# Optimization experiments

Hardware: AMD Instinct MI355X
Metric: run time of the kernel (lower is better)

Reference implementation:

```python
import jax, jax.numpy as jnp
import numpy as np

B, Q, DIN, DOUT = 1, 1024, 4096, 4096
H, G, HD = 32, 8, 128          # heads, kv groups, head_dim; group_size = H // G
PREV = 3072                     # cached KV length
MAXPOS = 4096                   # rope table length (>= PREV + Q)
START = PREV


def _rope_tables(max_pos, head_dim):
    half = head_dim // 2
    inv_freq = 1.0 / (10000.0 ** (jnp.arange(half, dtype=jnp.float32) / half))
    ang = jnp.arange(max_pos, dtype=jnp.float32)[:, None] * inv_freq[None, :]
    ang = jnp.concatenate([ang, ang], axis=-1)  # [max_pos, head_dim]
    return jnp.cos(ang), jnp.sin(ang)


def apply_rope(x, cos, sin, start_pos):
    # x: [b, h, s, d]; rotate-half RoPE with absolute positions start_pos..start_pos+s
    s, d = x.shape[2], x.shape[3]
    c = cos[start_pos:start_pos + s]  # [s, d] (start_pos is a Python int)
    sn = sin[start_pos:start_pos + s]
    x1, x2 = x[..., : d // 2], x[..., d // 2:]
    rotated = jnp.concatenate([-x2, x1], axis=-1)
    return x * c + rotated * sn


def setup_inputs() -> dict:
    key = jax.random.key(0)
    ks = jax.random.split(key, 7)
    x = jax.random.normal(ks[0], (B, Q, DIN), dtype=jnp.float32)
    cos, sin = _rope_tables(MAXPOS, HD)
    # causal mask: query at abs position START+i may attend kv position j <= START+i
    qpos = START + jnp.arange(Q)
    kpos = jnp.arange(START + Q)
    mask = (kpos[None, :] > qpos[:, None])[None, None]  # [1,1,Q,KV], True = masked
    prev_k = jax.random.normal(ks[1], (B, G, PREV, HD), dtype=jnp.float32)
    prev_v = jax.random.normal(ks[2], (B, G, PREV, HD), dtype=jnp.float32)
    sc = 0.02
    Wq = jax.random.normal(ks[3], (DIN, DOUT), dtype=jnp.float32) * sc
    Wk = jax.random.normal(ks[4], (DIN, G * HD), dtype=jnp.float32) * sc
    Wv = jax.random.normal(ks[5], (DIN, G * HD), dtype=jnp.float32) * sc
    Wo = jax.random.normal(ks[6], (DOUT, DOUT), dtype=jnp.float32) * sc
    return dict(x=x, mask=mask, cos=cos, sin=sin, start_pos=START,
                prev_k=prev_k, prev_v=prev_v, Wq=Wq, Wk=Wk, Wv=Wv, Wo=Wo)


def reference(x, mask, cos, sin, start_pos, prev_k, prev_v, Wq, Wk, Wv, Wo):
    b, s, _ = x.shape
    gs = H // G  # group_size
    q = (x @ Wq).reshape(b, s, H, HD).transpose(0, 2, 1, 3)   # [b,H,s,hd]
    k = (x @ Wk).reshape(b, s, G, HD).transpose(0, 2, 1, 3)   # [b,G,s,hd]
    v = (x @ Wv).reshape(b, s, G, HD).transpose(0, 2, 1, 3)
    q = apply_rope(q, cos, sin, start_pos)
    k = apply_rope(k, cos, sin, start_pos)
    keys = jnp.concatenate([prev_k, k], axis=2)    # [b,G,KV,hd]
    values = jnp.concatenate([prev_v, v], axis=2)
    # grouped attention (equivalent to repeat_interleave of K/V over group_size)
    qg = q.reshape(b, G, gs, s, HD)
    scores = jnp.einsum('bgnqd,bgkd->bgnqk', qg, keys)        # [b,G,gs,s,KV]
    scores = jnp.where(mask[:, :, None], -jnp.inf, scores)
    attn = jax.nn.softmax(scores / np.sqrt(HD).astype(np.float32), axis=-1)
    ctx = jnp.einsum('bgnqk,bgkd->bgnqd', attn, values)       # [b,G,gs,s,hd]
    ctx = ctx.reshape(b, H, s, HD).transpose(0, 2, 1, 3).reshape(b, s, DOUT)
    out = ctx @ Wo
    return (out, keys, values)
```

## Files before the change

### kernel.cpp

```cpp
#include <hip/hip_runtime.h>
#include <hip/hip_bf16.h>

typedef unsigned short u16;
typedef unsigned int u32;
typedef __attribute__((ext_vector_type(4))) float f32x4;
typedef __attribute__((ext_vector_type(16))) float f32x16;
typedef __attribute__((ext_vector_type(8))) __bf16 bf16x8;
typedef __attribute__((ext_vector_type(4))) u16 u16x4;
typedef __attribute__((ext_vector_type(8))) u16 u16x8;
typedef __attribute__((ext_vector_type(4))) u32 u32x4;

#define START_POS 3072
#define NKV 4096
#define HD_ 128
#define SEQ 1024
#define DIN_ 4096
#define DQKV 6144

__device__ __forceinline__ void gll16(const void* g, void* l) {
  __builtin_amdgcn_global_load_lds((const __attribute__((address_space(1))) u32*)g,
                                   (__attribute__((address_space(3))) u32*)l, 16, 0, 0);
}
__device__ __forceinline__ u16 f2bf(float f) {
  u32 u = __builtin_bit_cast(u32, f);
  return (u16)((u + 0x7fffu + ((u >> 16) & 1u)) >> 16);
}
__device__ __forceinline__ float bf2f(u16 u) {
  u32 x = (u32)u << 16;
  return __builtin_bit_cast(float, x);
}
__device__ __forceinline__ u32 pack2bf(float a, float b) {
  __hip_bfloat162 t = __float22bfloat162_rn(float2{a, b});
  u32 u; __builtin_memcpy(&u, &t, 4);
  return u;
}
__device__ __forceinline__ f32x4 mfma16(bf16x8 a, bf16x8 b, f32x4 c) {
  return __builtin_amdgcn_mfma_f32_16x16x32_bf16(a, b, c, 0, 0, 0);
}
__device__ __forceinline__ f32x16 mfma32(bf16x8 a, bf16x8 b, f32x16 c) {
  return __builtin_amdgcn_mfma_f32_32x32x16_bf16(a, b, c, 0, 0, 0);
}

__global__ __launch_bounds__(256) void wtrans(const float* __restrict__ W,
    u16* __restrict__ Wt, int N, int ntn, int row_off)
{
  __shared__ float T[64][68];
  int bid = blockIdx.x;
  int nt = bid % ntn, kt = bid / ntn;
  int t = threadIdx.x;
  int kl = t >> 4, nl4 = (t & 15) << 2;
#pragma unroll
  for (int r = 0; r < 4; r++) {
    int row = r * 16 + kl;
    f32x4 v = *(const f32x4*)(W + (size_t)(kt * 64 + row) * N + nt * 64 + nl4);
    T[row][nl4] = v[0]; T[row][nl4 + 1] = v[1]; T[row][nl4 + 2] = v[2]; T[row][nl4 + 3] = v[3];
  }
  __syncthreads();
  int nl = t >> 2, k0 = (t & 3) << 4;
  u16x8 lo, hi;
#pragma unroll
  for (int j = 0; j < 8; j++) lo[j] = f2bf(T[k0 + j][nl]);
#pragma unroll
  for (int j = 0; j < 8; j++) hi[j] = f2bf(T[k0 + 8 + j][nl]);
  u16* dst = Wt + (size_t)(row_off + nt * 64 + nl) * 4096 + kt * 64 + k0;
  *(u16x8*)dst = lo;
  *(u16x8*)(dst + 8) = hi;
}

__global__ __launch_bounds__(256) void cvt_bf16(const float* __restrict__ src,
    u16* __restrict__ dst, int n4)
{
  int i = blockIdx.x * 256 + threadIdx.x;
  if (i >= n4) return;
  f32x4 v = *(const f32x4*)(src + (size_t)i * 4);
  u16x4 o;
#pragma unroll
  for (int j = 0; j < 4; j++) o[j] = f2bf(v[j]);
  *(u16x4*)(dst + (size_t)i * 4) = o;
}

__global__ __launch_bounds__(256) void gemm_bt(
    const u16* __restrict__ A, const u16* __restrict__ Bt,
    float* __restrict__ C, int N, int K, int nbx)
{
  __shared__ u16 As[2 * 128 * 64];
  __shared__ u16 Bs[2 * 64 * 64];
  int nwg = (int)gridDim.x;
  int orig = blockIdx.x;
  int q8 = nwg >> 3, r8 = nwg & 7;
  int xcd = orig & 7, jj = orig >> 3;
  int wgid = (xcd < r8 ? xcd * (q8 + 1) : r8 * (q8 + 1) + (xcd - r8) * q8) + jj;
  int by = wgid / nbx, bx = wgid % nbx;
  int tid = threadIdx.x, lane = tid & 63, wid = tid >> 6;
  int wr = wid >> 1, wc = wid & 1;
  int c = lane & 15, hh = lane >> 4;
  int srow = lane >> 3;
  int schunk = ((lane & 7) ^ srow) << 3;
  const u16* aS0 = A + (size_t)(by * 128 + wid * 32 + srow) * K + schunk;
  const u16* bS0 = Bt + (size_t)(bx * 64 + wid * 16 + srow) * K + schunk;

#define GSTAGE(buf, kk) do { \
  _Pragma("unroll") \
  for (int r = 0; r < 4; r++) \
    gll16(aS0 + (size_t)r * 8 * K + (kk), As + (buf) * 8192 + (wid * 32 + r * 8) * 64); \
  _Pragma("unroll") \
  for (int r = 0; r < 2; r++) \
    gll16(bS0 + (size_t)r * 8 * K + (kk), Bs + (buf) * 4096 + (wid * 16 + r * 8) * 64); \
} while (0)

  f32x4 acc[4][2] = {};
  int nk = K >> 6;
  int cur = 0;
  int rsl = c & 7;
  GSTAGE(0, 0);
  __syncthreads();
  for (int kt = 0; kt < nk; kt++) {
    if (kt + 1 < nk) GSTAGE(cur ^ 1, (kt + 1) * 64);
    const u16* Ab = As + cur * 8192;
    const u16* Bb = Bs + cur * 4096;
#pragma unroll
    for (int kk = 0; kk < 2; kk++) {
      int slot = ((kk * 4 + hh) ^ rsl) * 8;
      bf16x8 af[4], bf[2];
#pragma unroll
      for (int i = 0; i < 4; i++)
        af[i] = *(const bf16x8*)(Ab + (wr * 64 + i * 16 + c) * 64 + slot);
#pragma unroll
      for (int i = 0; i < 2; i++)
        bf[i] = *(const bf16x8*)(Bb + (wc * 32 + i * 16 + c) * 64 + slot);
      __builtin_amdgcn_s_setprio(1);
#pragma unroll
      for (int mi = 0; mi < 4; mi++)
#pragma unroll
        for (int ni = 0; ni < 2; ni++)
          acc[mi][ni] = mfma16(af[mi], bf[ni], acc[mi][ni]);
      __builtin_amdgcn_s_setprio(0);
    }
    __syncthreads();
    cur ^= 1;
  }
#undef GSTAGE
  int row0 = by * 128 + wr * 64 + hh * 4;
  int col0 = bx * 64 + wc * 32 + c;
#pragma unroll
  for (int mi = 0; mi < 4; mi++)
#pragma unroll
    for (int ni = 0; ni < 2; ni++)
#pragma unroll
      for (int i = 0; i < 4; i++)
        C[(size_t)(row0 + mi * 16 + i) * N + col0 + ni * 16] = acc[mi][ni][i];
}

__global__ __launch_bounds__(256) void rope_q(const float* __restrict__ qkv,
    const float* __restrict__ cosb, const float* __restrict__ sinb, u16* __restrict__ qb)
{
  const float C2 = 0.12751744f;
  int tid = blockIdx.x * 256 + threadIdx.x;
  int dq = tid & 15, h = (tid >> 4) & 31, s = tid >> 9;
  int d = dq << 2;
  const float* base = qkv + (size_t)s * DQKV + h * HD_ + d;
  f32x4 a = *(const f32x4*)base;
  f32x4 b2 = *(const f32x4*)(base + 64);
  f32x4 cc = *(const f32x4*)(cosb + (size_t)(START_POS + s) * HD_ + d);
  f32x4 sn = *(const f32x4*)(sinb + (size_t)(START_POS + s) * HD_ + d);
  u16x4 o1, o2;
#pragma unroll
  for (int i = 0; i < 4; i++) {
    o1[i] = f2bf((a[i] * cc[i] - b2[i] * sn[i]) * C2);
    o2[i] = f2bf((b2[i] * cc[i] + a[i] * sn[i]) * C2);
  }
  u16* dst = qb + ((size_t)h * SEQ + s) * HD_ + d;
  *(u16x4*)dst = o1;
  *(u16x4*)(dst + 64) = o2;
}

__global__ __launch_bounds__(256) void rope_k(const float* __restrict__ qkv,
    const float* __restrict__ cosb, const float* __restrict__ sinb,
    float* __restrict__ keys, u16* __restrict__ kbb)
{
  int tid = blockIdx.x * 256 + threadIdx.x;
  int dq = tid & 15, g = (tid >> 4) & 7, s = tid >> 7;
  int d = dq << 2;
  const float* base = qkv + (size_t)s * DQKV + DIN_ + g * HD_ + d;
  f32x4 a = *(const f32x4*)base;
  f32x4 b2 = *(const f32x4*)(base + 64);
  f32x4 cc = *(const f32x4*)(cosb + (size_t)(START_POS + s) * HD_ + d);
  f32x4 sn = *(const f32x4*)(sinb + (size_t)(START_POS + s) * HD_ + d);
  f32x4 o1, o2;
  u16x4 p1, p2;
#pragma unroll
  for (int i = 0; i < 4; i++) {
    o1[i] = a[i] * cc[i] - b2[i] * sn[i];
    o2[i] = b2[i] * cc[i] + a[i] * sn[i];
    p1[i] = f2bf(o1[i]);
    p2[i] = f2bf(o2[i]);
  }
  size_t off = ((size_t)g * NKV + START_POS + s) * HD_ + d;
  *(f32x4*)(keys + off) = o1;
  *(f32x4*)(keys + off + 64) = o2;
  *(u16x4*)(kbb + off) = p1;
  *(u16x4*)(kbb + off + 64) = p2;
}

__global__ __launch_bounds__(256) void copy_vnew(const float* __restrict__ qkv,
    float* __restrict__ values)
{
  int tid = blockIdx.x * 256 + threadIdx.x;
  int dq = tid & 31, g = (tid >> 5) & 7, s = tid >> 8;
  int d = dq << 2;
  f32x4 v = *(const f32x4*)(qkv + (size_t)s * DQKV + DIN_ + 1024 + g * HD_ + d);
  *(f32x4*)(values + ((size_t)g * NKV + START_POS + s) * HD_ + d) = v;
}

__global__ __launch_bounds__(256) void prev_copy(const float* __restrict__ pk,
    const float* __restrict__ pv, float* __restrict__ keys, float* __restrict__ values,
    u16* __restrict__ kbb)
{
  int idx = blockIdx.x * 256 + threadIdx.x;
  int d4 = idx & 31;
  int rest = idx >> 5;
  int p = rest % 3072, g = rest / 3072;
  f32x4 kq = *(const f32x4*)(pk + (size_t)idx * 4);
  f32x4 vq = *(const f32x4*)(pv + (size_t)idx * 4);
  size_t off = ((size_t)g * NKV + p) * HD_ + d4 * 4;
  *(f32x4*)(keys + off) = kq;
  *(f32x4*)(values + off) = vq;
  u16x4 kb4;
#pragma unroll
  for (int i = 0; i < 4; i++) kb4[i] = f2bf(kq[i]);
  *(u16x4*)(kbb + off) = kb4;
}

__global__ __launch_bounds__(256) void vtrans(const float* __restrict__ pv,
    const float* __restrict__ qkv, u16* __restrict__ vT)
{
  __shared__ float T[64][68];
  int bid = blockIdx.x;
  int dt = bid & 1, pt = (bid >> 1) & 63, g = bid >> 7;
  int t = threadIdx.x;
  int pl = t >> 4, dl4 = (t & 15) << 2;
#pragma unroll
  for (int r = 0; r < 4; r++) {
    int row = r * 16 + pl;
    int pos = pt * 64 + row;
    f32x4 v;
    if (pos < START_POS)
      v = *(const f32x4*)(pv + ((size_t)g * START_POS + pos) * HD_ + dt * 64 + dl4);
    else
      v = *(const f32x4*)(qkv + (size_t)(pos - START_POS) * DQKV + 5120 + g * HD_ + dt * 64 + dl4);
    T[row][dl4] = v[0]; T[row][dl4 + 1] = v[1]; T[row][dl4 + 2] = v[2]; T[row][dl4 + 3] = v[3];
  }
  __syncthreads();
  int dl = t >> 2, p0 = (t & 3) << 4;
  u16x8 lo, hi;
#pragma unroll
  for (int j = 0; j < 8; j++) lo[j] = f2bf(T[p0 + j][dl]);
#pragma unroll
  for (int j = 0; j < 8; j++) hi[j] = f2bf(T[p0 + 8 + j][dl]);
  u16* dst = vT + ((size_t)g * HD_ + dt * 64 + dl) * NKV + pt * 64 + p0;
  *(u16x8*)dst = lo;
  *(u16x8*)(dst + 8) = hi;
}

__global__ __launch_bounds__(256, 2) void attn_fwd(
    const u16* __restrict__ qb, const u16* __restrict__ kb,
    const u16* __restrict__ vT, u16* __restrict__ Op, float* __restrict__ Ml)
{
  __shared__ u16 Ks[2 * 32 * 128];
  __shared__ u16 Vs[2 * 128 * 32];
  int bid = blockIdx.x;
  int g = bid & 7, j = bid >> 3;
  int sp = j >> 5, jj = j & 31;
  int h = g * 4 + (jj >> 3), qt = jj & 7;
  int tid = threadIdx.x, lane = tid & 63, w = tid >> 6;
  int c32 = lane & 31, h8 = lane >> 5;
  int qw0 = qt * 128 + w * 32;
  bf16x8 Qf[8];
#pragma unroll
  for (int dc = 0; dc < 8; dc++)
    Qf[dc] = *(const bf16x8*)(qb + ((size_t)(h * 1024 + qw0 + c32)) * 128 + dc * 16 + h8 * 8);
  f32x16 O0 = {}, O1 = {}, O2 = {}, O3 = {};
  float Mx = -1e30f, Ls = 0.f;
  int T = 100 + 4 * qt;
  int t0 = (sp * T) >> 2;
  int t1 = ((sp + 1) * T) >> 2;

#define STAGE_KV(tt, bo) do { \
  _Pragma("unroll") \
  for (int r = 0; r < 2; r++) { \
    int s = r * 256 + w * 64 + lane; \
    int krow = s >> 4, sl = s & 15; \
    gll16(kb + ((size_t)(g * 4096 + (tt) * 32 + krow)) * 128 + (sl ^ (krow & 7)) * 8, \
          Ks + (bo) + (r * 256 + w * 64) * 8); \
    int d = s >> 2, sl2 = s & 3; \
    gll16(vT + ((size_t)(g * 128 + d)) * 4096 + (tt) * 32 + (sl2 ^ ((d >> 1) & 3)) * 8, \
          Vs + (bo) + (r * 256 + w * 64) * 8); \
  } \
} while (0)

  int cur = 0;
  STAGE_KV(t0, 0);
  __syncthreads();
  int vxr = (c32 >> 1) & 3;
  for (int t = t0; t < t1; t++) {
    if (t + 1 < t1) STAGE_KV(t + 1, (cur ^ 1) * 4096);
    const u16* Kb = Ks + cur * 4096;
    const u16* Vb = Vs + cur * 4096;
    f32x16 S0 = {}, Sb = {};
    __builtin_amdgcn_s_setprio(1);
#pragma unroll
    for (int dc = 0; dc < 8; dc += 2) {
      int sxA = (2 * dc + h8) ^ (c32 & 7);
      int sxB = (2 * dc + 2 + h8) ^ (c32 & 7);
      bf16x8 kA = *(const bf16x8*)(Kb + (size_t)c32 * 128 + sxA * 8);
      bf16x8 kB = *(const bf16x8*)(Kb + (size_t)c32 * 128 + sxB * 8);
      S0 = mfma32(kA, Qf[dc], S0);
      Sb = mfma32(kB, Qf[dc + 1], Sb);
    }
    __builtin_amdgcn_s_setprio(0);
#pragma unroll
    for (int r = 0; r < 16; r++) S0[r] += Sb[r];
    if (t * 32 + 31 > START_POS + qw0) {
      int qa = START_POS + qw0 + c32;
#pragma unroll
      for (int r = 0; r < 16; r++) {
        int kvo = t * 32 + (r & 3) + 8 * (r >> 2) + 4 * h8;
        if (kvo > qa) S0[r] = -1e30f;
      }
    }
    float tm[16];
#pragma unroll
    for (int r = 0; r < 16; r++) tm[r] = S0[r];
#pragma unroll
    for (int sft = 8; sft >= 1; sft >>= 1)
#pragma unroll
      for (int r = 0; r < sft; r++) tm[r] = fmaxf(tm[r], tm[r + sft]);
    float full = fmaxf(tm[0], __shfl_xor(tm[0], 32));
    if (!__all(full <= Mx + 8.0f)) {
      float Mn = fmaxf(Mx, full);
      float al = exp2f(Mx - Mn);
      Mx = Mn;
      Ls *= al;
#pragma unroll
      for (int r = 0; r < 16; r++) { O0[r] *= al; O1[r] *= al; O2[r] *= al; O3[r] *= al; }
    }
#pragma unroll
    for (int r = 0; r < 16; r++) S0[r] = exp2f(S0[r] - Mx);
    float ts[16];
#pragma unroll
    for (int r = 0; r < 16; r++) ts[r] = S0[r];
#pragma unroll
    for (int sft = 8; sft >= 1; sft >>= 1)
#pragma unroll
      for (int r = 0; r < sft; r++) ts[r] = ts[r] + ts[r + sft];
    Ls += ts[0] + __shfl_xor(ts[0], 32);
    u32 pk0[8], x0[8];
#pragma unroll
    for (int m = 0; m < 8; m++) pk0[m] = pack2bf(S0[2 * m], S0[2 * m + 1]);
#pragma unroll
    for (int m = 0; m < 8; m++) x0[m] = __shfl_xor(pk0[m], 32);
    bf16x8 pbf[2];
    {
      u32x4 f0 = { h8 ? x0[2] : pk0[0], h8 ? x0[3] : pk0[1],
                   h8 ? pk0[2] : x0[0], h8 ? pk0[3] : x0[1] };
      u32x4 f1 = { h8 ? x0[6] : pk0[4], h8 ? x0[7] : pk0[5],
                   h8 ? pk0[6] : x0[4], h8 ? pk0[7] : x0[5] };
      pbf[0] = __builtin_bit_cast(bf16x8, f0);
      pbf[1] = __builtin_bit_cast(bf16x8, f1);
    }
    __builtin_amdgcn_s_setprio(1);
#pragma unroll
    for (int kc = 0; kc < 2; kc++) {
      int sv = 2 * kc + h8;
      int sx = (sv ^ vxr) * 8;
      {
        bf16x8 vf = *(const bf16x8*)(Vb + (size_t)(0 * 32 + c32) * 32 + sx);
        O0 = mfma32(vf, pbf[kc], O0);
      }
      {
        bf16x8 vf = *(const bf16x8*)(Vb + (size_t)(1 * 32 + c32) * 32 + sx);
        O1 = mfma32(vf, pbf[kc], O1);
      }
      {
        bf16x8 vf = *(const bf16x8*)(Vb + (size_t)(2 * 32 + c32) * 32 + sx);
        O2 = mfma32(vf, pbf[kc], O2);
      }
      {
        bf16x8 vf = *(const bf16x8*)(Vb + (size_t)(3 * 32 + c32) * 32 + sx);
        O3 = mfma32(vf, pbf[kc], O3);
      }
    }
    __builtin_amdgcn_s_setprio(0);
    __syncthreads();
    cur ^= 1;
  }
#undef STAGE_KV
  {
    u16* Orow = Op + (size_t)sp * 4194304 + (size_t)(qw0 + c32) * 4096 + h * 128;
#pragma unroll
    for (int a = 0; a < 4; a++) {
      u16x4 o0, o1, o2, o3;
#pragma unroll
      for (int b = 0; b < 4; b++) {
        o0[b] = f2bf(O0[4 * a + b]); o1[b] = f2bf(O1[4 * a + b]);
        o2[b] = f2bf(O2[4 * a + b]); o3[b] = f2bf(O3[4 * a + b]);
      }
      int d0 = 8 * a + 4 * h8;
      *(u16x4*)(Orow + d0) = o0;
      *(u16x4*)(Orow + 32 + d0) = o1;
      *(u16x4*)(Orow + 64 + d0) = o2;
      *(u16x4*)(Orow + 96 + d0) = o3;
    }
    if (h8 == 0) {
      float* mp = Ml + ((size_t)(sp * 32 + h) * 1024 + qw0 + c32) * 2;
      mp[0] = Mx; mp[1] = Ls;
    }
  }
}

__global__ __launch_bounds__(256) void attn_combine(const u16* __restrict__ Op,
    const float* __restrict__ Ml, u16* __restrict__ ctxb)
{
  int idx = blockIdx.x * 256 + threadIdx.x;
  int q = idx >> 10, c4 = idx & 1023;
  int col = c4 * 4, h = col >> 7;
  float m[4], l[4];
#pragma unroll
  for (int s = 0; s < 4; s++) {
    const float* mp = Ml + ((size_t)(s * 32 + h) * 1024 + q) * 2;
    m[s] = mp[0]; l[s] = mp[1];
  }
  float M = fmaxf(fmaxf(m[0], m[1]), fmaxf(m[2], m[3]));
  float wgt[4];
  float den = 0.f;
#pragma unroll
  for (int s = 0; s < 4; s++) { wgt[s] = exp2f(m[s] - M); den += l[s] * wgt[s]; }
  float inv = 1.0f / den;
  float acc[4] = {0.f, 0.f, 0.f, 0.f};
#pragma unroll
  for (int s = 0; s < 4; s++) {
    u16x4 raw = *(const u16x4*)(Op + (size_t)s * 4194304 + (size_t)q * 4096 + col);
#pragma unroll
    for (int i = 0; i < 4; i++) acc[i] += bf2f(raw[i]) * wgt[s];
  }
  u16x4 o;
#pragma unroll
  for (int i = 0; i < 4; i++) o[i] = f2bf(acc[i] * inv);
  *(u16x4*)(ctxb + (size_t)q * 4096 + col) = o;
}

extern "C" void kernel_launch(void* const* d_in, const int* in_sizes, int n_in,
                              void* d_out, int out_size, void* d_ws, size_t ws_size,
                              hipStream_t stream) {
  const float* x      = (const float*)d_in[0];
  const float* cosb   = (const float*)d_in[2];
  const float* sinb   = (const float*)d_in[3];
  const float* prev_k = (const float*)d_in[5];
  const float* prev_v = (const float*)d_in[6];
  const float* Wq     = (const float*)d_in[7];
  const float* Wk     = (const float*)d_in[8];
  const float* Wv     = (const float*)d_in[9];
  const float* Wo     = (const float*)d_in[10];

  u16* Wt_proj = (u16*)d_ws;
  u16* Wt_out  = Wt_proj + (size_t)6144 * 4096;
  u16* xb      = Wt_out + (size_t)4096 * 4096;
  float* qkv   = (float*)(xb + (size_t)1024 * 4096);
  u16* qb      = (u16*)(qkv + (size_t)1024 * 6144);
  u16* kbb     = qb + (size_t)32 * 1024 * 128;
  u16* vT      = kbb + (size_t)8 * 4096 * 128;
  u16* ctxb    = vT + (size_t)8 * 4096 * 128;
  u16* Op   = (u16*)d_ws;
  float* Ml = qkv;

  float* outp   = (float*)d_out;
  float* keys   = outp + (size_t)4194304;
  float* values = outp + (size_t)8388608;

  wtrans<<<4096, 256, 0, stream>>>(Wq, Wt_proj, 4096, 64, 0);
  wtrans<<<1024, 256, 0, stream>>>(Wk, Wt_proj, 1024, 16, 4096);
  wtrans<<<1024, 256, 0, stream>>>(Wv, Wt_proj, 1024, 16, 5120);
  wtrans<<<4096, 256, 0, stream>>>(Wo, Wt_out, 4096, 64, 0);
  cvt_bf16<<<4096, 256, 0, stream>>>(x, xb, 1048576);

  gemm_bt<<<768, 256, 0, stream>>>(xb, Wt_proj, qkv, 6144, 4096, 96);

  rope_q<<<2048, 256, 0, stream>>>(qkv, cosb, sinb, qb);
  rope_k<<<512, 256, 0, stream>>>(qkv, cosb, sinb, keys, kbb);
  copy_vnew<<<1024, 256, 0, stream>>>(qkv, values);
  prev_copy<<<3072, 256, 0, stream>>>(prev_k, prev_v, keys, values, kbb);
  vtrans<<<1024, 256, 0, stream>>>(prev_v, qkv, vT);

  attn_fwd<<<1024, 256, 0, stream>>>(qb, kbb, vT, Op, Ml);
  attn_combine<<<4096, 256, 0, stream>>>(Op, Ml, ctxb);

  gemm_bt<<<512, 256, 0, stream>>>(ctxb, Wt_out, outp, 4096, 4096, 64);
}
```

Baseline: 342.5 us.

## Software-pipeline attention loop so next QK^T overlaps softmax and PV

Restructures the flash-attention main loop so each iteration issues the PV accumulation for the previous tile, runs softmax for the current tile, then computes QK^T for the next tile after the barrier. This lets MFMA work overlap softmax's VALU and transcendental work within a wave. To keep the V tile of the previous step alive while the next one is being staged, V moves to a triple buffer, which adds 8 KB of LDS per block. It also keeps more accumulators live, which raises register pressure. The prologue assumes each split has at least two KV tiles.

```diff
diff --git a/kernel.cpp b/kernel.cpp
--- a/kernel.cpp
+++ b/kernel.cpp
@@ -267,7 +267,7 @@
     const u16* __restrict__ vT, u16* __restrict__ Op, float* __restrict__ Ml)
 {
   __shared__ u16 Ks[2 * 32 * 128];
-  __shared__ u16 Vs[2 * 128 * 32];
+  __shared__ u16 Vs[3 * 128 * 32];
   int bid = blockIdx.x;
   int g = bid & 7, j = bid >> 3;
   int sp = j >> 5, jj = j & 31;
@@ -285,116 +285,142 @@
   int t0 = (sp * T) >> 2;
   int t1 = ((sp + 1) * T) >> 2;
 
-#define STAGE_KV(tt, bo) do { \
+#define STAGE_K(tt, bo) do { \
   _Pragma("unroll") \
   for (int r = 0; r < 2; r++) { \
     int s = r * 256 + w * 64 + lane; \
     int krow = s >> 4, sl = s & 15; \
     gll16(kb + ((size_t)(g * 4096 + (tt) * 32 + krow)) * 128 + (sl ^ (krow & 7)) * 8, \
           Ks + (bo) + (r * 256 + w * 64) * 8); \
+  } \
+} while (0)
+#define STAGE_V(tt, bo) do { \
+  _Pragma("unroll") \
+  for (int r = 0; r < 2; r++) { \
+    int s = r * 256 + w * 64 + lane; \
     int d = s >> 2, sl2 = s & 3; \
     gll16(vT + ((size_t)(g * 128 + d)) * 4096 + (tt) * 32 + (sl2 ^ ((d >> 1) & 3)) * 8, \
           Vs + (bo) + (r * 256 + w * 64) * 8); \
   } \
 } while (0)
 
-  int cur = 0;
-  STAGE_KV(t0, 0);
+#define QKT(SS, kbase) do { \
+  f32x16 s0_ = {}, sb_ = {}; \
+  __builtin_amdgcn_s_setprio(1); \
+  _Pragma("unroll") \
+  for (int dc = 0; dc < 8; dc += 2) { \
+    int sxA_ = (2 * dc + h8) ^ (c32 & 7); \
+    int sxB_ = (2 * dc + 2 + h8) ^ (c32 & 7); \
+    bf16x8 kA_ = *(const bf16x8*)((kbase) + (size_t)c32 * 128 + sxA_ * 8); \
+    bf16x8 kB_ = *(const bf16x8*)((kbase) + (size_t)c32 * 128 + sxB_ * 8); \
+    s0_ = mfma32(kA_, Qf[dc], s0_); \
+    sb_ = mfma32(kB_, Qf[dc + 1], sb_); \
+  } \
+  __builtin_amdgcn_s_setprio(0); \
+  _Pragma("unroll") \
+  for (int r = 0; r < 16; r++) SS[r] = s0_[r] + sb_[r]; \
+} while (0)
+
+#define PVACC(PB, vbase) do { \
+  __builtin_amdgcn_s_setprio(1); \
+  _Pragma("unroll") \
+  for (int kc = 0; kc < 2; kc++) { \
+    int sx_ = ((2 * kc + h8) ^ vxr) * 8; \
+    O0 = mfma32(*(const bf16x8*)((vbase) + (size_t)(0 * 32 + c32) * 32 + sx_), PB[kc], O0); \
+    O1 = mfma32(*(const bf16x8*)((vbase) + (size_t)(1 * 32 + c32) * 32 + sx_), PB[kc], O1); \
+    O2 = mfma32(*(const bf16x8*)((vbase) + (size_t)(2 * 32 + c32) * 32 + sx_), PB[kc], O2); \
+    O3 = mfma32(*(const bf16x8*)((vbase) + (size_t)(3 * 32 + c32) * 32 + sx_), PB[kc], O3); \
+  } \
+  __builtin_amdgcn_s_setprio(0); \
+} while (0)
+
+#define SOFTMAX(tt, SS, NPB) do { \
+  if ((tt) * 32 + 31 > START_POS + qw0) { \
+    int qa_ = START_POS + qw0 + c32; \
+    _Pragma("unroll") \
+    for (int r = 0; r < 16; r++) { \
+      int kvo_ = (tt) * 32 + (r & 3) + 8 * (r >> 2) + 4 * h8; \
+      if (kvo_ > qa_) SS[r] = -1e30f; \
+    } \
+  } \
+  float tm_[16]; \
+  _Pragma("unroll") \
+  for (int r = 0; r < 16; r++) tm_[r] = SS[r]; \
+  _Pragma("unroll") \
+  for (int sft = 8; sft >= 1; sft >>= 1) \
+    _Pragma("unroll") \
+    for (int r = 0; r < sft; r++) tm_[r] = fmaxf(tm_[r], tm_[r + sft]); \
+  float full_ = fmaxf(tm_[0], __shfl_xor(tm_[0], 32)); \
+  if (!__all(full_ <= Mx + 8.0f)) { \
+    float Mn_ = fmaxf(Mx, full_); \
+    float al_ = exp2f(Mx - Mn_); \
+    Mx = Mn_; Ls *= al_; \
+    _Pragma("unroll") \
+    for (int r = 0; r < 16; r++) { O0[r] *= al_; O1[r] *= al_; O2[r] *= al_; O3[r] *= al_; } \
+  } \
+  _Pragma("unroll") \
+  for (int r = 0; r < 16; r++) SS[r] = exp2f(SS[r] - Mx); \
+  float ts_[16]; \
+  _Pragma("unroll") \
+  for (int r = 0; r < 16; r++) ts_[r] = SS[r]; \
+  _Pragma("unroll") \
+  for (int sft = 8; sft >= 1; sft >>= 1) \
+    _Pragma("unroll") \
+    for (int r = 0; r < sft; r++) ts_[r] = ts_[r] + ts_[r + sft]; \
+  Ls += ts_[0] + __shfl_xor(ts_[0], 32); \
+  u32 pk_[8], x_[8]; \
+  _Pragma("unroll") \
+  for (int m = 0; m < 8; m++) pk_[m] = pack2bf(SS[2 * m], SS[2 * m + 1]); \
+  _Pragma("unroll") \
+  for (int m = 0; m < 8; m++) x_[m] = __shfl_xor(pk_[m], 32); \
+  { \
+    u32x4 f0_ = { h8 ? x_[2] : pk_[0], h8 ? x_[3] : pk_[1], \
+                  h8 ? pk_[2] : x_[0], h8 ? pk_[3] : x_[1] }; \
+    u32x4 f1_ = { h8 ? x_[6] : pk_[4], h8 ? x_[7] : pk_[5], \
+                  h8 ? pk_[6] : x_[4], h8 ? pk_[7] : x_[5] }; \
+    NPB[0] = __builtin_bit_cast(bf16x8, f0_); \
+    NPB[1] = __builtin_bit_cast(bf16x8, f1_); \
+  } \
+} while (0)
+
+  int vxr = (c32 >> 1) & 3;
+  STAGE_K(t0, 0);
+  STAGE_V(t0, 0);
   __syncthreads();
-  int vxr = (c32 >> 1) & 3;
-  for (int t = t0; t < t1; t++) {
-    if (t + 1 < t1) STAGE_KV(t + 1, (cur ^ 1) * 4096);
-    const u16* Kb = Ks + cur * 4096;
-    const u16* Vb = Vs + cur * 4096;
-    f32x16 S0 = {}, Sb = {};
-    __builtin_amdgcn_s_setprio(1);
-#pragma unroll
-    for (int dc = 0; dc < 8; dc += 2) {
-      int sxA = (2 * dc + h8) ^ (c32 & 7);
-      int sxB = (2 * dc + 2 + h8) ^ (c32 & 7);
-      bf16x8 kA = *(const bf16x8*)(Kb + (size_t)c32 * 128 + sxA * 8);
-      bf16x8 kB = *(const bf16x8*)(Kb + (size_t)c32 * 128 + sxB * 8);
-      S0 = mfma32(kA, Qf[dc], S0);
-      Sb = mfma32(kB, Qf[dc + 1], Sb);
+  f32x16 S;
+  QKT(S, Ks);
+  bf16x8 pA[2];
+  {
+    STAGE_K(t0 + 1, 4096);
+    STAGE_V(t0 + 1, 4096);
+    SOFTMAX(t0, S, pA);
+    __syncthreads();
+    QKT(S, Ks + 4096);
+  }
+  int cur = 1, vb = 1;
+  for (int t = t0 + 1; t < t1; t++) {
+    bool nxt = (t + 1 < t1);
+    if (nxt) {
+      STAGE_K(t + 1, (cur ^ 1) * 4096);
+      STAGE_V(t + 1, ((vb + 1) % 3) * 4096);
     }
-    __builtin_amdgcn_s_setprio(0);
-#pragma unroll
-    for (int r = 0; r < 16; r++) S0[r] += Sb[r];
-    if (t * 32 + 31 > START_POS + qw0) {
-      int qa = START_POS + qw0 + c32;
-#pragma unroll
-      for (int r = 0; r < 16; r++) {
-        int kvo = t * 32 + (r & 3) + 8 * (r >> 2) + 4 * h8;
-        if (kvo > qa) S0[r] = -1e30f;
-      }
+    PVACC(pA, Vs + ((vb + 2) % 3) * 4096);
+    bf16x8 pN[2];
+    SOFTMAX(t, S, pN);
+    pA[0] = pN[0]; pA[1] = pN[1];
+    if (nxt) {
+      __syncthreads();
+      QKT(S, Ks + (cur ^ 1) * 4096);
+      cur ^= 1;
+      vb = (vb + 1) % 3;
     }
-    float tm[16];
-#pragma unroll
-    for (int r = 0; r < 16; r++) tm[r] = S0[r];
-#pragma unroll
-    for (int sft = 8; sft >= 1; sft >>= 1)
-#pragma unroll
-      for (int r = 0; r < sft; r++) tm[r] = fmaxf(tm[r], tm[r + sft]);
-    float full = fmaxf(tm[0], __shfl_xor(tm[0], 32));
-    if (!__all(full <= Mx + 8.0f)) {
-      float Mn = fmaxf(Mx, full);
-      float al = exp2f(Mx - Mn);
-      Mx = Mn;
-      Ls *= al;
-#pragma unroll
-      for (int r = 0; r < 16; r++) { O0[r] *= al; O1[r] *= al; O2[r] *= al; O3[r] *= al; }
-    }
-#pragma unroll
-    for (int r = 0; r < 16; r++) S0[r] = exp2f(S0[r] - Mx);
-    float ts[16];
-#pragma unroll
-    for (int r = 0; r < 16; r++) ts[r] = S0[r];
-#pragma unroll
-    for (int sft = 8; sft >= 1; sft >>= 1)
-#pragma unroll
-      for (int r = 0; r < sft; r++) ts[r] = ts[r] + ts[r + sft];
-    Ls += ts[0] + __shfl_xor(ts[0], 32);
-    u32 pk0[8], x0[8];
-#pragma unroll
-    for (int m = 0; m < 8; m++) pk0[m] = pack2bf(S0[2 * m], S0[2 * m + 1]);
-#pragma unroll
-    for (int m = 0; m < 8; m++) x0[m] = __shfl_xor(pk0[m], 32);
-    bf16x8 pbf[2];
-    {
-      u32x4 f0 = { h8 ? x0[2] : pk0[0], h8 ? x0[3] : pk0[1],
-                   h8 ? pk0[2] : x0[0], h8 ? pk0[3] : x0[1] };
-      u32x4 f1 = { h8 ? x0[6] : pk0[4], h8 ? x0[7] : pk0[5],
-                   h8 ? pk0[6] : x0[4], h8 ? pk0[7] : x0[5] };
-      pbf[0] = __builtin_bit_cast(bf16x8, f0);
-      pbf[1] = __builtin_bit_cast(bf16x8, f1);
-    }
-    __builtin_amdgcn_s_setprio(1);
-#pragma unroll
-    for (int kc = 0; kc < 2; kc++) {
-      int sv = 2 * kc + h8;
-      int sx = (sv ^ vxr) * 8;
-      {
-        bf16x8 vf = *(const bf16x8*)(Vb + (size_t)(0 * 32 + c32) * 32 + sx);
-        O0 = mfma32(vf, pbf[kc], O0);
-      }
-      {
-        bf16x8 vf = *(const bf16x8*)(Vb + (size_t)(1 * 32 + c32) * 32 + sx);
-        O1 = mfma32(vf, pbf[kc], O1);
-      }
-      {
-        bf16x8 vf = *(const bf16x8*)(Vb + (size_t)(2 * 32 + c32) * 32 + sx);
-        O2 = mfma32(vf, pbf[kc], O2);
-      }
-      {
-        bf16x8 vf = *(const bf16x8*)(Vb + (size_t)(3 * 32 + c32) * 32 + sx);
-        O3 = mfma32(vf, pbf[kc], O3);
-      }
-    }
-    __builtin_amdgcn_s_setprio(0);
-    __syncthreads();
-    cur ^= 1;
-  }
-#undef STAGE_KV
+  }
+  PVACC(pA, Vs + vb * 4096);
+#undef STAGE_K
+#undef STAGE_V
+#undef QKT
+#undef PVACC
+#undef SOFTMAX
   {
     u16* Orow = Op + (size_t)sp * 4194304 + (size_t)(qw0 + c32) * 4096 + h * 128;
 #pragma unroll
```

New measurement: 334.3 us. -2.4%, faster.
